# Optimization experiments

Measured on AMD Instinct MI355X. Metric: run time of the kernel, lower is better.

## Reference

```python
import jax, jax.numpy as jnp
import numpy as np


def _layernorm(x, w, b):
    mu = x.mean(-1, keepdims=True)
    var = ((x - mu) ** 2).mean(-1, keepdims=True)
    return (x - mu) * jax.lax.rsqrt(var + 1e-5) * w + b


def _s5_scan(u, Lam, Bc, Cc, D, log_step):
    # Diagonal S5 SSM, ZOH discretization, parallel associative scan over time.
    step = jnp.exp(log_step)                       # (P,)
    Lbar = jnp.exp(Lam * step)                     # (P,) complex
    Bbar = ((Lbar - 1.0) / Lam)[:, None] * Bc      # (P,H) complex
    Bu = jnp.einsum('ph,blh->blp', Bbar, u.astype(Bbar.dtype))  # (B,L,P)
    Le = jnp.broadcast_to(Lbar, Bu.shape)

    def binop(e1, e2):
        a1, b1 = e1
        a2, b2 = e2
        return a1 * a2, a2 * b1 + b2

    _, xs = jax.lax.associative_scan(binop, (Le, Bu), axis=1)   # hidden states (B,L,P)
    return 2.0 * jnp.einsum('hp,blp->blh', Cc, xs).real + D * u


def _s5_block(x, ln1_w, ln1_b, Lam_re, Lam_im, B_re, B_im, C_re, C_im, D, log_step,
              ln2_w, ln2_b, ff_enc_w, ff_dec_w):
    # S5Block.forward (dropout = identity at inference)
    fx = _layernorm(x, ln1_w, ln1_b)
    Lam = -jnp.exp(Lam_re) + 1j * Lam_im           # stable-real parametrization
    y = _s5_scan(fx, Lam, B_re + 1j * B_im, C_re + 1j * C_im, D, log_step)
    x = jax.nn.gelu(y, approximate=False) + fx
    fx = _layernorm(x, ln2_w, ln2_b)
    h = fx @ ff_enc_w                              # (B,L,2N) -> GEGLU
    v, g = jnp.split(h, 2, axis=-1)
    h = v * jax.nn.gelu(g, approximate=False)
    return h @ ff_dec_w + fx


def reference(z_input, dt, ln1_w, ln1_b, Lam_re, Lam_im, B_re, B_im, C_re, C_im, D,
              log_step, ln2_w, ln2_b, ff_enc_w, ff_dec_w, toA_w1, toA_b1, toA_w2,
              toA_b2, mask_A):
    Bsz, L, N = z_input.shape
    x = z_input
    for i in range(ln1_w.shape[0]):                # n_ssmlayer_A stacked S5 blocks
        x = _s5_block(x, ln1_w[i], ln1_b[i], Lam_re[i], Lam_im[i], B_re[i], B_im[i],
                      C_re[i], C_im[i], D[i], log_step[i], ln2_w[i], ln2_b[i],
                      ff_enc_w[i], ff_dec_w[i])
    # ssm_to_A: Linear -> Softplus -> Linear
    h = jax.nn.softplus(x @ toA_w1 + toA_b1)
    Unk_A = h @ toA_w2 + toA_b2                    # (B,L,N*N)
    # SSM_step_ODE.get_seq_dynamics with A_known_const = 0
    A = Unk_A.reshape(Bsz, L, N, N) * mask_A
    # bilinear (Tustin) discretization: A_bar = (I - dt/2 A)^-1 (I + dt/2 A)
    I = jnp.eye(N, dtype=A.dtype)
    dtA = 0.5 * dt[..., None, None] * A
    A_bar = jnp.linalg.solve(I - dtA, I + dtA)     # (B,L,N,N)
    # roll latent state through the discretized dynamics
    z0 = z_input[:, 0]

    def step(z, Ab):
        z2 = jnp.einsum('bij,bj->bi', Ab, z)
        return z2, z2

    _, ys = jax.lax.scan(step, z0, jnp.moveaxis(A_bar[:, :-1], 1, 0))
    traj = jnp.concatenate([z0[None], ys], axis=0)  # (L,B,N)
    return jnp.moveaxis(traj, 0, 1)                 # (B,L,N)


def setup_inputs() -> dict:
    key = jax.random.key(0)
    ks = jax.random.split(key, 16)
    B, L, N, P, NL, H = 32, 512, 64, 128, 2, 128
    d = {}
    d['z_input'] = jax.random.normal(ks[0], (B, L, N), jnp.float32)
    d['dt'] = jax.random.uniform(ks[1], (B, L), jnp.float32) * 0.01
    d['ln1_w'] = jnp.ones((NL, N), jnp.float32)
    d['ln1_b'] = jnp.zeros((NL, N), jnp.float32)
    d['Lam_re'] = jax.random.normal(ks[2], (NL, P), jnp.float32) * 0.5
    d['Lam_im'] = jax.random.normal(ks[3], (NL, P), jnp.float32) * np.pi
    d['B_re'] = jax.random.normal(ks[4], (NL, P, N), jnp.float32) / np.sqrt(N)
    d['B_im'] = jax.random.normal(ks[5], (NL, P, N), jnp.float32) / np.sqrt(N)
    d['C_re'] = jax.random.normal(ks[6], (NL, N, P), jnp.float32) / np.sqrt(P)
    d['C_im'] = jax.random.normal(ks[7], (NL, N, P), jnp.float32) / np.sqrt(P)
    d['D'] = jax.random.normal(ks[8], (NL, N), jnp.float32)
    lo, hi = np.log(1e-3), np.log(1e-1)
    d['log_step'] = lo + jax.random.uniform(ks[9], (NL, P), jnp.float32) * (hi - lo)
    d['ln2_w'] = jnp.ones((NL, N), jnp.float32)
    d['ln2_b'] = jnp.zeros((NL, N), jnp.float32)
    d['ff_enc_w'] = jax.random.normal(ks[10], (NL, N, 2 * N), jnp.float32) / np.sqrt(N)
    d['ff_dec_w'] = jax.random.normal(ks[11], (NL, N, N), jnp.float32) / np.sqrt(N)
    d['toA_w1'] = jax.random.normal(ks[12], (N, H), jnp.float32) * 0.1
    d['toA_b1'] = jnp.zeros((H,), jnp.float32)
    d['toA_w2'] = jax.random.normal(ks[13], (H, N * N), jnp.float32) * 0.002
    d['toA_b2'] = jnp.zeros((N * N,), jnp.float32)
    d['mask_A'] = jnp.ones((N, N), jnp.float32)
    return d
```

## Files before the change

### kernel.cpp

```cpp
#include <hip/hip_runtime.h>

#define DI __device__ __forceinline__

typedef unsigned short u16;
typedef unsigned int u32;
typedef __attribute__((ext_vector_type(8))) short shortx8;
typedef __attribute__((ext_vector_type(4))) float floatx4;

DI float u2f(u32 x) { union { u32 u; float f; } v; v.u = x; return v.f; }
DI u32 f2u(float x) { union { u32 u; float f; } v; v.f = x; return v.u; }
DI float bflo(u32 w) { return u2f(w << 16); }
DI float bfhi(u32 w) { return u2f(w & 0xffff0000u); }
DI float bf1(u16 w) { return u2f(((u32)w) << 16); }
DI u16 f2bf(float f) {
  u32 u = f2u(f);
  u32 r = (u + 0x7fffu + ((u >> 16) & 1u)) >> 16;
  return (u16)r;
}

DI float wsum64(float v) {
  v += __shfl_xor(v, 32);
  v += __shfl_xor(v, 16);
  v += __shfl_xor(v, 8);
  v += __shfl_xor(v, 4);
  v += __shfl_xor(v, 2);
  v += __shfl_xor(v, 1);
  return v;
}

DI float gelu_ex(float y) { return 0.5f * y * (1.0f + erff(y * 0.7071067811865476f)); }
DI float softplus_ex(float x) { return x > 0.f ? x + log1pf(expf(-x)) : log1pf(expf(x)); }

__global__ void k_pre(const float* __restrict__ Lam_re, const float* __restrict__ Lam_im,
                      const float* __restrict__ log_step,
                      const float* __restrict__ B_re, const float* __restrict__ B_im,
                      const float* __restrict__ C_re, const float* __restrict__ C_im,
                      float* __restrict__ wLbar, float* __restrict__ wBbr, float* __restrict__ wBbi,
                      float* __restrict__ wCtr, float* __restrict__ wCti) {
  int l = blockIdx.x;
  int p = threadIdx.x;
  int idx = l * 128 + p;
  float step = expf(log_step[idx]);
  float lre = -expf(Lam_re[idx]);
  float lim = Lam_im[idx];
  float er = expf(lre * step);
  float Lr = er * cosf(lim * step);
  float Li = er * sinf(lim * step);
  wLbar[idx * 2] = Lr;
  wLbar[idx * 2 + 1] = Li;
  float inv = 1.0f / (lre * lre + lim * lim);
  float nr = Lr - 1.0f, ni = Li;
  float qr = (nr * lre + ni * lim) * inv;
  float qi = (ni * lre - nr * lim) * inv;
  for (int h = 0; h < 64; ++h) {
    float br = B_re[idx * 64 + h], bim = B_im[idx * 64 + h];
    wBbr[(l * 64 + h) * 128 + p] = qr * br - qi * bim;
    wBbi[(l * 64 + h) * 128 + p] = qr * bim + qi * br;
    wCtr[idx * 64 + h] = C_re[(l * 64 + h) * 128 + p];
    wCti[idx * 64 + h] = C_im[(l * 64 + h) * 128 + p];
  }
}

__global__ __launch_bounds__(256) void k_prew(const float* __restrict__ w2, u16* __restrict__ w2T) {
  __shared__ float s[128][65];
  int t = threadIdx.x;
  int n0 = blockIdx.x * 64;
  for (int i = 0; i < 32; ++i) {
    int e = i * 256 + t;
    int k = e >> 6, n = e & 63;
    s[k][n] = w2[(size_t)k * 4096 + n0 + n];
  }
  __syncthreads();
  for (int i = 0; i < 16; ++i) {
    int e = i * 256 + t;
    int n = e >> 6, kp = e & 63;
    u32 pk = (u32)f2bf(s[kp * 2][n]) | ((u32)f2bf(s[kp * 2 + 1][n]) << 16);
    ((u32*)w2T)[(size_t)(n0 + n) * 64 + kp] = pk;
  }
}

__global__ __launch_bounds__(256) void k_ln_bu(
    const float* __restrict__ xin, const float* __restrict__ lnw, const float* __restrict__ lnb,
    const float* __restrict__ wBbr, const float* __restrict__ wBbi,
    float* __restrict__ fxg, float2* __restrict__ bu, int layer) {
  __shared__ float sbr[64 * 128];
  __shared__ float sbi[64 * 128];
  int t = threadIdx.x, w = t >> 6, lane = t & 63;
  {
    const float* br = wBbr + (size_t)layer * 8192;
    const float* bi = wBbi + (size_t)layer * 8192;
    for (int e = t; e < 8192; e += 256) { sbr[e] = br[e]; sbi[e] = bi[e]; }
  }
  float wv = lnw[layer * 64 + lane], bv = lnb[layer * 64 + lane];
  __syncthreads();
  int row0 = blockIdx.x * 32 + w * 8;
  float fxv[8];
#pragma unroll
  for (int rr = 0; rr < 8; ++rr) {
    size_t r = row0 + rr;
    float x = xin[r * 64 + lane];
    float mu = wsum64(x) * 0.015625f;
    float d = x - mu;
    float var = wsum64(d * d) * 0.015625f;
    float fx = d * rsqrtf(var + 1e-5f) * wv + bv;
    fxv[rr] = fx;
    fxg[r * 64 + lane] = fx;
  }
  float ar0[8] = {}, ai0[8] = {}, ar1[8] = {}, ai1[8] = {};
  for (int h = 0; h < 64; ++h) {
    float b0r = sbr[h * 128 + lane], b0i = sbi[h * 128 + lane];
    float b1r = sbr[h * 128 + lane + 64], b1i = sbi[h * 128 + lane + 64];
#pragma unroll
    for (int rr = 0; rr < 8; ++rr) {
      float f = __shfl(fxv[rr], h);
      ar0[rr] = fmaf(b0r, f, ar0[rr]);
      ai0[rr] = fmaf(b0i, f, ai0[rr]);
      ar1[rr] = fmaf(b1r, f, ar1[rr]);
      ai1[rr] = fmaf(b1i, f, ai1[rr]);
    }
  }
#pragma unroll
  for (int rr = 0; rr < 8; ++rr) {
    size_t r = row0 + rr;
    bu[r * 128 + lane] = make_float2(ar0[rr], ai0[rr]);
    bu[r * 128 + lane + 64] = make_float2(ar1[rr], ai1[rr]);
  }
}

__global__ __launch_bounds__(256) void k_scan(float2* __restrict__ bu,
                                              const float* __restrict__ wLbar, int layer) {
  __shared__ float2 carry[16][17];
  int t = threadIdx.x;
  int ck = t >> 4, chain = t & 15;
  int b = blockIdx.x >> 3;
  int p = (blockIdx.x & 7) * 16 + chain;
  float Lr = wLbar[(layer * 128 + p) * 2];
  float Li = wLbar[(layer * 128 + p) * 2 + 1];
  float2* ptr = bu + ((size_t)b * 512 * 128 + p);
  int l0 = ck * 32;
  float xr = 0.f, xi = 0.f;
#pragma unroll 4
  for (int i = 0; i < 32; ++i) {
    float2 v = ptr[(size_t)(l0 + i) * 128];
    float nr = fmaf(Lr, xr, fmaf(-Li, xi, v.x));
    float ni = fmaf(Lr, xi, fmaf(Li, xr, v.y));
    xr = nr; xi = ni;
  }
  carry[chain][ck] = make_float2(xr, xi);
  __syncthreads();
  if (t < 16) {
    float ar = Lr, ai = Li;
#pragma unroll
    for (int s = 0; s < 5; ++s) {
      float nr = ar * ar - ai * ai;
      float ni = 2.f * ar * ai;
      ar = nr; ai = ni;
    }
    float cr = 0.f, ci2 = 0.f;
#pragma unroll
    for (int m = 0; m < 16; ++m) {
      float2 loc = carry[t][m];
      carry[t][m] = make_float2(cr, ci2);
      float nr = fmaf(ar, cr, fmaf(-ai, ci2, loc.x));
      float ni = fmaf(ar, ci2, fmaf(ai, cr, loc.y));
      cr = nr; ci2 = ni;
    }
  }
  __syncthreads();
  float2 c0 = carry[chain][ck];
  xr = c0.x; xi = c0.y;
#pragma unroll 4
  for (int i = 0; i < 32; ++i) {
    float2 v = ptr[(size_t)(l0 + i) * 128];
    float nr = fmaf(Lr, xr, fmaf(-Li, xi, v.x));
    float ni = fmaf(Lr, xi, fmaf(Li, xr, v.y));
    xr = nr; xi = ni;
    ptr[(size_t)(l0 + i) * 128] = make_float2(xr, xi);
  }
}

__global__ __launch_bounds__(256) void k_yproj(
    const float2* __restrict__ xs, const float* __restrict__ wCtr, const float* __restrict__ wCti,
    const float* __restrict__ fxg, const float* __restrict__ Dp,
    float* __restrict__ xout, int layer) {
  __shared__ float ctr[64 * 64];
  __shared__ float cti[64 * 64];
  __shared__ float2 xsh[4][8][64];
  int t = threadIdx.x, w = t >> 6, lane = t & 63;
  int row0 = blockIdx.x * 32 + w * 8;
  float acc[8] = {};
  for (int ph = 0; ph < 2; ++ph) {
    __syncthreads();
    {
      const float* sr = wCtr + ((size_t)layer * 128 + ph * 64) * 64;
      const float* si = wCti + ((size_t)layer * 128 + ph * 64) * 64;
      for (int e = t; e < 4096; e += 256) { ctr[e] = sr[e]; cti[e] = si[e]; }
    }
#pragma unroll
    for (int rr = 0; rr < 8; ++rr) {
      size_t r = row0 + rr;
      xsh[w][rr][lane] = xs[r * 128 + ph * 64 + lane];
    }
    __syncthreads();
    for (int p = 0; p < 64; ++p) {
      float cr = ctr[p * 64 + lane];
      float ci = cti[p * 64 + lane];
#pragma unroll
      for (int rr = 0; rr < 8; ++rr) {
        float2 xv = xsh[w][rr][p];
        acc[rr] = fmaf(cr, xv.x, fmaf(-ci, xv.y, acc[rr]));
      }
    }
  }
  float Dv = Dp[layer * 64 + lane];
#pragma unroll
  for (int rr = 0; rr < 8; ++rr) {
    size_t r = row0 + rr;
    float u = fxg[r * 64 + lane];
    float y = 2.f * acc[rr] + Dv * u;
    xout[r * 64 + lane] = gelu_ex(y) + u;
  }
}

__global__ __launch_bounds__(256) void k_ff(
    float* __restrict__ xio, const float* __restrict__ lnw, const float* __restrict__ lnb,
    const float* __restrict__ encw, const float* __restrict__ decw, int layer) {
  __shared__ float enc[64 * 128];
  __shared__ float dec[64 * 64];
  int t = threadIdx.x, w = t >> 6, lane = t & 63;
  {
    const float* e = encw + (size_t)layer * 8192;
    for (int i = t; i < 8192; i += 256) enc[i] = e[i];
    const float* d = decw + (size_t)layer * 4096;
    for (int i = t; i < 4096; i += 256) dec[i] = d[i];
  }
  float wv = lnw[layer * 64 + lane], bv = lnb[layer * 64 + lane];
  __syncthreads();
  int row0 = blockIdx.x * 32 + w * 8;
  float fx2v[8];
#pragma unroll
  for (int rr = 0; rr < 8; ++rr) {
    size_t r = row0 + rr;
    float x = xio[r * 64 + lane];
    float mu = wsum64(x) * 0.015625f;
    float d = x - mu;
    float var = wsum64(d * d) * 0.015625f;
    fx2v[rr] = d * rsqrtf(var + 1e-5f) * wv + bv;
  }
  float h0[8] = {}, h1v[8] = {};
  for (int h = 0; h < 64; ++h) {
    float e0 = enc[h * 128 + lane], e1 = enc[h * 128 + lane + 64];
#pragma unroll
    for (int rr = 0; rr < 8; ++rr) {
      float f = __shfl(fx2v[rr], h);
      h0[rr] = fmaf(e0, f, h0[rr]);
      h1v[rr] = fmaf(e1, f, h1v[rr]);
    }
  }
  float gv[8];
#pragma unroll
  for (int rr = 0; rr < 8; ++rr) gv[rr] = h0[rr] * gelu_ex(h1v[rr]);
  float o[8] = {};
  for (int j = 0; j < 64; ++j) {
    float dv = dec[j * 64 + lane];
#pragma unroll
    for (int rr = 0; rr < 8; ++rr) {
      float gj = __shfl(gv[rr], j);
      o[rr] = fmaf(dv, gj, o[rr]);
    }
  }
#pragma unroll
  for (int rr = 0; rr < 8; ++rr) {
    size_t r = row0 + rr;
    xio[r * 64 + lane] = o[rr] + fx2v[rr];
  }
}

__global__ __launch_bounds__(256) void k_toa1(
    const float* __restrict__ xin, const float* __restrict__ w1, const float* __restrict__ b1,
    u16* __restrict__ h1out) {
  __shared__ float w1s[64 * 128];
  int t = threadIdx.x, w = t >> 6, lane = t & 63;
  for (int i = t; i < 8192; i += 256) w1s[i] = w1[i];
  float bb0 = b1[lane], bb1 = b1[lane + 64];
  __syncthreads();
  int row0 = blockIdx.x * 32 + w * 8;
  float xv[8];
#pragma unroll
  for (int rr = 0; rr < 8; ++rr) xv[rr] = xin[(size_t)(row0 + rr) * 64 + lane];
  float a0[8] = {}, a1[8] = {};
  for (int h = 0; h < 64; ++h) {
    float e0 = w1s[h * 128 + lane], e1 = w1s[h * 128 + lane + 64];
#pragma unroll
    for (int rr = 0; rr < 8; ++rr) {
      float f = __shfl(xv[rr], h);
      a0[rr] = fmaf(e0, f, a0[rr]);
      a1[rr] = fmaf(e1, f, a1[rr]);
    }
  }
#pragma unroll
  for (int rr = 0; rr < 8; ++rr) {
    size_t r = row0 + rr;
    float v0 = softplus_ex(a0[rr] + bb0);
    float v1 = softplus_ex(a1[rr] + bb1);
    int sl = (2 * lane) & 63;
    float ea = __shfl(v0, sl), eb = __shfl(v1, sl);
    float oa = __shfl(v0, sl + 1), ob = __shfl(v1, sl + 1);
    float lo = (lane < 32) ? ea : eb;
    float hi = (lane < 32) ? oa : ob;
    ((u32*)h1out)[r * 64 + lane] = (u32)f2bf(lo) | ((u32)f2bf(hi) << 16);
  }
}

__global__ __launch_bounds__(256) void k_gemm_mfma(
    const u16* __restrict__ w2T,
    const u16* __restrict__ h1,
    const float* __restrict__ b2, const float* __restrict__ mask,
    const float* __restrict__ dt, u16* __restrict__ Xout) {
  __shared__ __align__(16) u16 As[128 * 128];
  __shared__ __align__(16) u16 Bs[128 * 128];
  int t = threadIdx.x;
  int bn = blockIdx.x;
  int bm = blockIdx.y;
  {
    const u16* srcA = w2T + (size_t)(bn * 128) * 128;
    const u16* srcB = h1 + (size_t)(bm * 128) * 128;
#pragma unroll
    for (int i = 0; i < 8; ++i) {
      int r = i * 16 + (t >> 4);
      int gs = t & 15;
      int gsw = (gs & 8) | ((gs ^ r) & 7);
      uint4 va = *(const uint4*)(srcA + r * 128 + gs * 8);
      *(uint4*)(As + r * 128 + gsw * 8) = va;
      uint4 vb = *(const uint4*)(srcB + r * 128 + gs * 8);
      *(uint4*)(Bs + r * 128 + gsw * 8) = vb;
    }
  }
  __syncthreads();
  int w = t >> 6, l = t & 63;
  int n0 = (w & 1) * 64, m0 = (w >> 1) * 64;
  int lr = l & 15, kg = l >> 4;
  floatx4 acc[4][4];
#pragma unroll
  for (int i = 0; i < 4; ++i)
#pragma unroll
    for (int j = 0; j < 4; ++j) acc[i][j] = (floatx4){0.f, 0.f, 0.f, 0.f};
#pragma unroll
  for (int kk = 0; kk < 4; ++kk) {
    int g = kk * 4 + kg;
    shortx8 af[4], bf[4];
#pragma unroll
    for (int ni = 0; ni < 4; ++ni) {
      int r = n0 + ni * 16 + lr;
      int gsw = (g & 8) | ((g ^ r) & 7);
      af[ni] = *(const shortx8*)(As + r * 128 + gsw * 8);
    }
#pragma unroll
    for (int mi = 0; mi < 4; ++mi) {
      int r = m0 + mi * 16 + lr;
      int gsw = (g & 8) | ((g ^ r) & 7);
      bf[mi] = *(const shortx8*)(Bs + r * 128 + gsw * 8);
    }
#pragma unroll
    for (int ni = 0; ni < 4; ++ni)
#pragma unroll
      for (int mi = 0; mi < 4; ++mi)
        acc[ni][mi] = __builtin_amdgcn_mfma_f32_16x16x32_bf16(af[ni], bf[mi], acc[ni][mi], 0, 0, 0);
  }
  __syncthreads();
  int q = (l >> 4) * 4;
#pragma unroll
  for (int mi = 0; mi < 4; ++mi) {
    int ml = m0 + mi * 16 + lr;
    int m = bm * 128 + ml;
    float dv = 0.5f * dt[m];
#pragma unroll
    for (int ni = 0; ni < 4; ++ni) {
      int nl = n0 + ni * 16 + q;
      int n = bn * 128 + nl;
      float4 bb = *(const float4*)&b2[n];
      float4 mk = *(const float4*)&mask[n];
      floatx4 a = acc[ni][mi];
      float x0 = dv * (a[0] + bb.x) * mk.x;
      float x1 = dv * (a[1] + bb.y) * mk.y;
      float x2 = dv * (a[2] + bb.z) * mk.z;
      float x3 = dv * (a[3] + bb.w) * mk.w;
      u32 lo = (u32)f2bf(x0) | ((u32)f2bf(x1) << 16);
      u32 hi = (u32)f2bf(x2) | ((u32)f2bf(x3) << 16);
      int g = nl >> 3;
      int gsw = (g & 8) | ((g ^ ml) & 7);
      *(uint2*)(As + ml * 128 + gsw * 8 + (nl & 7)) = make_uint2(lo, hi);
    }
  }
  __syncthreads();
  int seg = t & 7;
#pragma unroll
  for (int pp = 0; pp < 4; ++pp) {
    int r = pp * 32 + (t >> 3);
#pragma unroll
    for (int ii = 0; ii < 2; ++ii) {
      int g = seg * 2 + ii;
      int gsw = (g & 8) | ((g ^ r) & 7);
      uint4 v = *(const uint4*)(As + r * 128 + gsw * 8);
      *(uint4*)&Xout[(size_t)(bm * 128 + r) * 4096 + bn * 128 + g * 8] = v;
    }
  }
}

__global__ __launch_bounds__(256, 4) void k_chunk(u16* __restrict__ Xg) {
  __shared__ __align__(16) u16 Xrm[4096];
  __shared__ __align__(16) u16 XTrm[4096];
  __shared__ __align__(16) u16 Erm[4096];
  __shared__ __align__(16) u16 STb[4096];
  __shared__ __align__(16) u16 SOut[4096];
  int t = threadIdx.x, w = t >> 6, l = t & 63;
  int lr = l & 15, kg = l >> 4;
  int b = blockIdx.x >> 5, c = blockIdx.x & 31;
  u16* base = Xg + ((size_t)(b * 512 + c * 16)) * 4096;
  floatx4 sreg[4];
#pragma unroll
  for (int i = 0; i < 4; ++i) sreg[i] = (floatx4){0.f, 0.f, 0.f, 0.f};
  int r0 = (t >> 3) * 2, c0 = (t & 7) * 8, g0 = t & 7;
  int cw = t >> 3;
  uint4 pf0 = *(const uint4*)(base + r0 * 64 + c0);
  uint4 pf1 = *(const uint4*)(base + (r0 + 1) * 64 + c0);
  int q0 = w * 16 + kg * 4;
  int qrow = w * 16 + lr;
  int wr = t >> 2, wg = (t & 3) * 2;
  for (int j = 0; j < 16; ++j) {
    __syncthreads();
    if (j > 0) {
      u16* Xprev = base + (size_t)(j - 1) * 4096;
      uint4 v0 = *(const uint4*)(SOut + wr * 64 + (((wg + 0) ^ wr) & 7) * 8);
      uint4 v1 = *(const uint4*)(SOut + wr * 64 + (((wg + 1) ^ wr) & 7) * 8);
      *(uint4*)(Xprev + wr * 64 + wg * 8) = v0;
      *(uint4*)(Xprev + wr * 64 + wg * 8 + 8) = v1;
    }
    *(uint4*)(Xrm + r0 * 64 + ((g0 ^ r0) & 7) * 8) = pf0;
    *(uint4*)(Xrm + (r0 + 1) * 64 + ((g0 ^ (r0 + 1)) & 7) * 8) = pf1;
    {
      const u16* a = (const u16*)&pf0;
      const u16* bq = (const u16*)&pf1;
#pragma unroll
      for (int i = 0; i < 8; ++i) {
        int ci = (i + t) & 7;
        int cc = c0 + ci;
        u32 val = (u32)a[ci] | ((u32)bq[ci] << 16);
        ((u32*)XTrm)[cc * 32 + (((cw >> 2) ^ cc) & 7) * 4 + (cw & 3)] = val;
      }
    }
#pragma unroll
    for (int j2 = 0; j2 < 4; ++j2) {
      int p = j2 * 16 + lr;
      floatx4 s = sreg[j2];
      float v0 = s[0] + ((p == q0 + 0) ? 1.f : 0.f);
      float v1 = s[1] + ((p == q0 + 1) ? 1.f : 0.f);
      float v2 = s[2] + ((p == q0 + 2) ? 1.f : 0.f);
      float v3 = s[3] + ((p == q0 + 3) ? 1.f : 0.f);
      u32 lo = (u32)f2bf(v0) | ((u32)f2bf(v1) << 16);
      u32 hi = (u32)f2bf(v2) | ((u32)f2bf(v3) << 16);
      *(uint2*)(STb + p * 64 + (((q0 >> 3) ^ p) & 7) * 8 + (q0 & 7)) = make_uint2(lo, hi);
    }
    if (j < 15) {
      const u16* nx = base + (size_t)(j + 1) * 4096;
      pf0 = *(const uint4*)(nx + r0 * 64 + c0);
      pf1 = *(const uint4*)(nx + (r0 + 1) * 64 + c0);
    }
    __syncthreads();
    shortx8 afx0 = *(const shortx8*)(XTrm + qrow * 64 + ((kg ^ qrow) & 7) * 8);
    shortx8 afx1 = *(const shortx8*)(XTrm + qrow * 64 + (((4 + kg) ^ qrow) & 7) * 8);
    {
      floatx4 acc[4];
#pragma unroll
      for (int i = 0; i < 4; ++i) acc[i] = (floatx4){0.f, 0.f, 0.f, 0.f};
#pragma unroll
      for (int kk = 0; kk < 2; ++kk) {
        int g = kk * 4 + kg;
        shortx8 af = kk ? afx1 : afx0;
#pragma unroll
        for (int j2 = 0; j2 < 4; ++j2) {
          int p = j2 * 16 + lr;
          shortx8 bf = *(const shortx8*)(Xrm + p * 64 + ((g ^ p) & 7) * 8);
          acc[j2] = __builtin_amdgcn_mfma_f32_16x16x32_bf16(af, bf, acc[j2], 0, 0, 0);
        }
      }
#pragma unroll
      for (int j2 = 0; j2 < 4; ++j2) {
        int p = j2 * 16 + lr;
        int sw = (((q0 >> 3) ^ p) & 7) * 8 + (q0 & 7);
        uint2 xv = *(const uint2*)(Xrm + p * 64 + sw);
        floatx4 a = acc[j2];
        float e0 = 2.f * (bflo(xv.x) + a[0]);
        float e1 = 2.f * (bfhi(xv.x) + a[1]);
        float e2 = 2.f * (bflo(xv.y) + a[2]);
        float e3 = 2.f * (bfhi(xv.y) + a[3]);
        u32 lo = (u32)f2bf(e0) | ((u32)f2bf(e1) << 16);
        u32 hi = (u32)f2bf(e2) | ((u32)f2bf(e3) << 16);
        *(uint2*)(Erm + p * 64 + sw) = make_uint2(lo, hi);
      }
    }
    __syncthreads();
    {
      floatx4 acc[4];
#pragma unroll
      for (int i = 0; i < 4; ++i) acc[i] = (floatx4){0.f, 0.f, 0.f, 0.f};
#pragma unroll
      for (int kk = 0; kk < 2; ++kk) {
        int g = kk * 4 + kg;
        shortx8 af = *(const shortx8*)(Erm + qrow * 64 + ((g ^ qrow) & 7) * 8);
#pragma unroll
        for (int j2 = 0; j2 < 4; ++j2) {
          int p = j2 * 16 + lr;
          shortx8 bf = *(const shortx8*)(STb + p * 64 + ((g ^ p) & 7) * 8);
          acc[j2] = __builtin_amdgcn_mfma_f32_16x16x32_bf16(af, bf, acc[j2], 0, 0, 0);
        }
      }
#pragma unroll
      for (int j2 = 0; j2 < 4; ++j2) {
        int p = j2 * 16 + lr;
        floatx4 a = acc[j2];
        floatx4 s = sreg[j2];
        s[0] += a[0]; s[1] += a[1]; s[2] += a[2]; s[3] += a[3];
        sreg[j2] = s;
        u32 lo = (u32)f2bf(s[0]) | ((u32)f2bf(s[1]) << 16);
        u32 hi = (u32)f2bf(s[2]) | ((u32)f2bf(s[3]) << 16);
        *(uint2*)(SOut + p * 64 + (((q0 >> 3) ^ p) & 7) * 8 + (q0 & 7)) = make_uint2(lo, hi);
      }
    }
  }
  __syncthreads();
  {
    u16* Xprev = base + (size_t)15 * 4096;
    uint4 v0 = *(const uint4*)(SOut + wr * 64 + (((wg + 0) ^ wr) & 7) * 8);
    uint4 v1 = *(const uint4*)(SOut + wr * 64 + (((wg + 1) ^ wr) & 7) * 8);
    *(uint4*)(Xprev + wr * 64 + wg * 8) = v0;
    *(uint4*)(Xprev + wr * 64 + wg * 8 + 8) = v1;
  }
}

__global__ __launch_bounds__(64) void k_carry(const float* __restrict__ zin,
                                              const u16* __restrict__ R,
                                              float* __restrict__ out) {
  __shared__ __align__(16) u16 Ms[2][4096];
  int b = blockIdx.x, l = threadIdx.x;
  {
    const u16* M0 = R + ((size_t)(b * 512 + 15)) * 4096;
#pragma unroll
    for (int i = 0; i < 8; ++i) ((uint4*)Ms[0])[i * 64 + l] = ((const uint4*)M0)[i * 64 + l];
  }
  float cz = zin[(size_t)b * 512 * 64 + l];
  for (int c = 0; c < 32; ++c) {
    out[((size_t)(b * 512 + c * 16)) * 64 + l] = cz;
    uint4 nf0, nf1, nf2, nf3, nf4, nf5, nf6, nf7;
    if (c < 31) {
      const u16* Mn = R + ((size_t)(b * 512 + (c + 1) * 16 + 15)) * 4096;
      nf0 = ((const uint4*)Mn)[0 * 64 + l];
      nf1 = ((const uint4*)Mn)[1 * 64 + l];
      nf2 = ((const uint4*)Mn)[2 * 64 + l];
      nf3 = ((const uint4*)Mn)[3 * 64 + l];
      nf4 = ((const uint4*)Mn)[4 * 64 + l];
      nf5 = ((const uint4*)Mn)[5 * 64 + l];
      nf6 = ((const uint4*)Mn)[6 * 64 + l];
      nf7 = ((const uint4*)Mn)[7 * 64 + l];
    }
    const u16* M = Ms[c & 1];
    float a0 = 0.f, a1 = 0.f, a2 = 0.f, a3 = 0.f;
#pragma unroll
    for (int k = 0; k < 64; k += 4) {
      a0 = fmaf(bf1(M[(k + 0) * 64 + l]), __shfl(cz, k + 0), a0);
      a1 = fmaf(bf1(M[(k + 1) * 64 + l]), __shfl(cz, k + 1), a1);
      a2 = fmaf(bf1(M[(k + 2) * 64 + l]), __shfl(cz, k + 2), a2);
      a3 = fmaf(bf1(M[(k + 3) * 64 + l]), __shfl(cz, k + 3), a3);
    }
    cz += (a0 + a1) + (a2 + a3);
    if (c < 31) {
      uint4* d = (uint4*)Ms[(c + 1) & 1];
      d[0 * 64 + l] = nf0; d[1 * 64 + l] = nf1; d[2 * 64 + l] = nf2; d[3 * 64 + l] = nf3;
      d[4 * 64 + l] = nf4; d[5 * 64 + l] = nf5; d[6 * 64 + l] = nf6; d[7 * 64 + l] = nf7;
    }
  }
}

__global__ __launch_bounds__(256) void k_apply(const u16* __restrict__ R,
                                               float* __restrict__ out) {
  __shared__ float carr[64];
  int t = threadIdx.x, w = t >> 6, l = t & 63;
  int b = blockIdx.x >> 5, c = blockIdx.x & 31;
  const u16* Rb = R + ((size_t)(b * 512 + c * 16)) * 4096;
  if (t < 64) carr[t] = out[((size_t)(b * 512 + c * 16)) * 64 + t];
  __syncthreads();
  for (int j = w; j < 15; j += 4) {
    const u16* M = Rb + (size_t)j * 4096;
    float a0 = 0.f, a1 = 0.f, a2 = 0.f, a3 = 0.f;
#pragma unroll
    for (int k = 0; k < 64; k += 4) {
      a0 = fmaf(bf1(M[(k + 0) * 64 + l]), carr[k + 0], a0);
      a1 = fmaf(bf1(M[(k + 1) * 64 + l]), carr[k + 1], a1);
      a2 = fmaf(bf1(M[(k + 2) * 64 + l]), carr[k + 2], a2);
      a3 = fmaf(bf1(M[(k + 3) * 64 + l]), carr[k + 3], a3);
    }
    float zo = carr[l] + ((a0 + a1) + (a2 + a3));
    out[((size_t)(b * 512 + c * 16 + j + 1)) * 64 + l] = zo;
  }
}

extern "C" void kernel_launch(void* const* d_in, const int* in_sizes, int n_in,
                              void* d_out, int out_size, void* d_ws, size_t ws_size,
                              hipStream_t stream) {
  const float* z_input  = (const float*)d_in[0];
  const float* dt       = (const float*)d_in[1];
  const float* ln1_w    = (const float*)d_in[2];
  const float* ln1_b    = (const float*)d_in[3];
  const float* Lam_re   = (const float*)d_in[4];
  const float* Lam_im   = (const float*)d_in[5];
  const float* B_re     = (const float*)d_in[6];
  const float* B_im     = (const float*)d_in[7];
  const float* C_re     = (const float*)d_in[8];
  const float* C_im     = (const float*)d_in[9];
  const float* Dp       = (const float*)d_in[10];
  const float* log_step = (const float*)d_in[11];
  const float* ln2_w    = (const float*)d_in[12];
  const float* ln2_b    = (const float*)d_in[13];
  const float* ff_enc   = (const float*)d_in[14];
  const float* ff_dec   = (const float*)d_in[15];
  const float* toA_w1   = (const float*)d_in[16];
  const float* toA_b1   = (const float*)d_in[17];
  const float* toA_w2   = (const float*)d_in[18];
  const float* toA_b2   = (const float*)d_in[19];
  const float* mask_A   = (const float*)d_in[20];

  char* ws = (char*)d_ws;
  float* wLbar = (float*)(ws + 0);
  float* wBbr  = (float*)(ws + 2048);
  float* wBbi  = (float*)(ws + 67584);
  float* wCtr  = (float*)(ws + 133120);
  float* wCti  = (float*)(ws + 198656);
  float* wfx   = (float*)(ws + 264192);
  float* wx    = (float*)(ws + 4458496);
  float2* wbu  = (float2*)(ws + 8652800);
  u16* wh1     = (u16*)(ws + 25430016);
  u16* w2T     = (u16*)(ws + 29624320);
  u16* wX      = (u16*)(ws + 30672896);
  if (ws_size < 164890624ull) return;

  k_pre<<<2, 128, 0, stream>>>(Lam_re, Lam_im, log_step, B_re, B_im, C_re, C_im,
                               wLbar, wBbr, wBbi, wCtr, wCti);
  k_prew<<<64, 256, 0, stream>>>(toA_w2, w2T);
  for (int l = 0; l < 2; ++l) {
    const float* xin = (l == 0) ? z_input : wx;
    k_ln_bu<<<512, 256, 0, stream>>>(xin, ln1_w, ln1_b, wBbr, wBbi, wfx, wbu, l);
    k_scan<<<256, 256, 0, stream>>>(wbu, wLbar, l);
    k_yproj<<<512, 256, 0, stream>>>(wbu, wCtr, wCti, wfx, Dp, wx, l);
    k_ff<<<512, 256, 0, stream>>>(wx, ln2_w, ln2_b, ff_enc, ff_dec, l);
  }
  k_toa1<<<512, 256, 0, stream>>>(wx, toA_w1, toA_b1, wh1);
  k_gemm_mfma<<<dim3(32, 128), 256, 0, stream>>>(w2T, wh1, toA_b2, mask_A, dt, wX);
  k_chunk<<<1024, 256, 0, stream>>>(wX);
  k_carry<<<32, 64, 0, stream>>>(z_input, wX, (float*)d_out);
  k_apply<<<1024, 256, 0, stream>>>(wX, (float*)d_out);
}
```

Before: 396.9 us.

## Fuse y-projection, feed-forward and toA1 kernels; merge prep kernels; register-resident carry matrices

Merges the two preprocessing kernels into one launch. Fuses the y-projection, FF block and (for the last layer) the first toA linear layer into a single kernel, with a shared-memory union. This removes intermediate global round-trips and several launches. The carry and apply kernels now read matrices with row-wise vector loads into registers instead of staging through shared memory, and the chunk kernel's output store is changed from packed to scalar transposed writes, which changes the stored layout and could slow that store path.

New measurement: 387.0 us. 1.03x faster.

```diff
diff --git a/kernel.cpp b/kernel.cpp
--- a/kernel.cpp
+++ b/kernel.cpp
@@ -31,51 +31,55 @@
 DI float gelu_ex(float y) { return 0.5f * y * (1.0f + erff(y * 0.7071067811865476f)); }
 DI float softplus_ex(float x) { return x > 0.f ? x + log1pf(expf(-x)) : log1pf(expf(x)); }
 
-__global__ void k_pre(const float* __restrict__ Lam_re, const float* __restrict__ Lam_im,
-                      const float* __restrict__ log_step,
-                      const float* __restrict__ B_re, const float* __restrict__ B_im,
-                      const float* __restrict__ C_re, const float* __restrict__ C_im,
-                      float* __restrict__ wLbar, float* __restrict__ wBbr, float* __restrict__ wBbi,
-                      float* __restrict__ wCtr, float* __restrict__ wCti) {
-  int l = blockIdx.x;
-  int p = threadIdx.x;
-  int idx = l * 128 + p;
-  float step = expf(log_step[idx]);
-  float lre = -expf(Lam_re[idx]);
-  float lim = Lam_im[idx];
-  float er = expf(lre * step);
-  float Lr = er * cosf(lim * step);
-  float Li = er * sinf(lim * step);
-  wLbar[idx * 2] = Lr;
-  wLbar[idx * 2 + 1] = Li;
-  float inv = 1.0f / (lre * lre + lim * lim);
-  float nr = Lr - 1.0f, ni = Li;
-  float qr = (nr * lre + ni * lim) * inv;
-  float qi = (ni * lre - nr * lim) * inv;
-  for (int h = 0; h < 64; ++h) {
-    float br = B_re[idx * 64 + h], bim = B_im[idx * 64 + h];
-    wBbr[(l * 64 + h) * 128 + p] = qr * br - qi * bim;
-    wBbi[(l * 64 + h) * 128 + p] = qr * bim + qi * br;
-    wCtr[idx * 64 + h] = C_re[(l * 64 + h) * 128 + p];
-    wCti[idx * 64 + h] = C_im[(l * 64 + h) * 128 + p];
-  }
-}
-
-__global__ __launch_bounds__(256) void k_prew(const float* __restrict__ w2, u16* __restrict__ w2T) {
-  __shared__ float s[128][65];
-  int t = threadIdx.x;
-  int n0 = blockIdx.x * 64;
-  for (int i = 0; i < 32; ++i) {
-    int e = i * 256 + t;
-    int k = e >> 6, n = e & 63;
-    s[k][n] = w2[(size_t)k * 4096 + n0 + n];
-  }
-  __syncthreads();
-  for (int i = 0; i < 16; ++i) {
-    int e = i * 256 + t;
-    int n = e >> 6, kp = e & 63;
-    u32 pk = (u32)f2bf(s[kp * 2][n]) | ((u32)f2bf(s[kp * 2 + 1][n]) << 16);
-    ((u32*)w2T)[(size_t)(n0 + n) * 64 + kp] = pk;
+__global__ __launch_bounds__(256) void k_pre2(
+    const float* __restrict__ Lam_re, const float* __restrict__ Lam_im,
+    const float* __restrict__ log_step,
+    const float* __restrict__ B_re, const float* __restrict__ B_im,
+    const float* __restrict__ C_re, const float* __restrict__ C_im,
+    const float* __restrict__ w2,
+    float* __restrict__ wLbar, float* __restrict__ wBbr, float* __restrict__ wBbi,
+    float* __restrict__ wCtr, float* __restrict__ wCti, u16* __restrict__ w2T) {
+  if (blockIdx.x < 64) {
+    __shared__ float s[128][65];
+    int t = threadIdx.x;
+    int n0 = blockIdx.x * 64;
+    for (int i = 0; i < 32; ++i) {
+      int e = i * 256 + t;
+      int k = e >> 6, n = e & 63;
+      s[k][n] = w2[(size_t)k * 4096 + n0 + n];
+    }
+    __syncthreads();
+    for (int i = 0; i < 16; ++i) {
+      int e = i * 256 + t;
+      int n = e >> 6, kp = e & 63;
+      u32 pk = (u32)f2bf(s[kp * 2][n]) | ((u32)f2bf(s[kp * 2 + 1][n]) << 16);
+      ((u32*)w2T)[(size_t)(n0 + n) * 64 + kp] = pk;
+    }
+  } else {
+    int l = blockIdx.x - 64;
+    int p = threadIdx.x;
+    if (p < 128) {
+      int idx = l * 128 + p;
+      float step = expf(log_step[idx]);
+      float lre = -expf(Lam_re[idx]);
+      float lim = Lam_im[idx];
+      float er = expf(lre * step);
+      float Lr = er * cosf(lim * step);
+      float Li = er * sinf(lim * step);
+      wLbar[idx * 2] = Lr;
+      wLbar[idx * 2 + 1] = Li;
+      float inv = 1.0f / (lre * lre + lim * lim);
+      float nr = Lr - 1.0f, ni = Li;
+      float qr = (nr * lre + ni * lim) * inv;
+      float qi = (ni * lre - nr * lim) * inv;
+      for (int h = 0; h < 64; ++h) {
+        float br = B_re[idx * 64 + h], bim = B_im[idx * 64 + h];
+        wBbr[(l * 64 + h) * 128 + p] = qr * br - qi * bim;
+        wBbi[(l * 64 + h) * 128 + p] = qr * bim + qi * br;
+        wCtr[idx * 64 + h] = C_re[(l * 64 + h) * 128 + p];
+        wCti[idx * 64 + h] = C_im[(l * 64 + h) * 128 + p];
+      }
+    }
   }
 }
 
@@ -179,13 +183,18 @@
   }
 }
 
-__global__ __launch_bounds__(256) void k_yproj(
+__global__ __launch_bounds__(256) void k_yff(
     const float2* __restrict__ xs, const float* __restrict__ wCtr, const float* __restrict__ wCti,
     const float* __restrict__ fxg, const float* __restrict__ Dp,
-    float* __restrict__ xout, int layer) {
-  __shared__ float ctr[64 * 64];
-  __shared__ float cti[64 * 64];
-  __shared__ float2 xsh[4][8][64];
+    const float* __restrict__ ln2w, const float* __restrict__ ln2b,
+    const float* __restrict__ encw, const float* __restrict__ decw,
+    const float* __restrict__ w1, const float* __restrict__ b1,
+    float* __restrict__ xout, u16* __restrict__ h1out, int layer) {
+  __shared__ union {
+    struct { float ctr[4096]; float cti[4096]; float2 xsh[4][8][64]; } a;
+    struct { float enc[8192]; float dec[4096]; } b;
+    struct { float w1s[8192]; } c;
+  } sm;
   int t = threadIdx.x, w = t >> 6, lane = t & 63;
   int row0 = blockIdx.x * 32 + w * 8;
   float acc[8] = {};
@@ -194,54 +203,46 @@
     {
       const float* sr = wCtr + ((size_t)layer * 128 + ph * 64) * 64;
       const float* si = wCti + ((size_t)layer * 128 + ph * 64) * 64;
-      for (int e = t; e < 4096; e += 256) { ctr[e] = sr[e]; cti[e] = si[e]; }
+      for (int e = t; e < 4096; e += 256) { sm.a.ctr[e] = sr[e]; sm.a.cti[e] = si[e]; }
     }
 #pragma unroll
     for (int rr = 0; rr < 8; ++rr) {
       size_t r = row0 + rr;
-      xsh[w][rr][lane] = xs[r * 128 + ph * 64 + lane];
+      sm.a.xsh[w][rr][lane] = xs[r * 128 + ph * 64 + lane];
     }
     __syncthreads();
     for (int p = 0; p < 64; ++p) {
-      float cr = ctr[p * 64 + lane];
-      float ci = cti[p * 64 + lane];
+      float cr = sm.a.ctr[p * 64 + lane];
+      float ci = sm.a.cti[p * 64 + lane];
 #pragma unroll
       for (int rr = 0; rr < 8; ++rr) {
-        float2 xv = xsh[w][rr][p];
+        float2 xv = sm.a.xsh[w][rr][p];
         acc[rr] = fmaf(cr, xv.x, fmaf(-ci, xv.y, acc[rr]));
       }
     }
   }
   float Dv = Dp[layer * 64 + lane];
+  float xv[8];
 #pragma unroll
   for (int rr = 0; rr < 8; ++rr) {
     size_t r = row0 + rr;
     float u = fxg[r * 64 + lane];
     float y = 2.f * acc[rr] + Dv * u;
-    xout[r * 64 + lane] = gelu_ex(y) + u;
-  }
-}
-
-__global__ __launch_bounds__(256) void k_ff(
-    float* __restrict__ xio, const float* __restrict__ lnw, const float* __restrict__ lnb,
-    const float* __restrict__ encw, const float* __restrict__ decw, int layer) {
-  __shared__ float enc[64 * 128];
-  __shared__ float dec[64 * 64];
-  int t = threadIdx.x, w = t >> 6, lane = t & 63;
+    xv[rr] = gelu_ex(y) + u;
+  }
+  __syncthreads();
   {
     const float* e = encw + (size_t)layer * 8192;
-    for (int i = t; i < 8192; i += 256) enc[i] = e[i];
+    for (int i = t; i < 8192; i += 256) sm.b.enc[i] = e[i];
     const float* d = decw + (size_t)layer * 4096;
-    for (int i = t; i < 4096; i += 256) dec[i] = d[i];
-  }
-  float wv = lnw[layer * 64 + lane], bv = lnb[layer * 64 + lane];
-  __syncthreads();
-  int row0 = blockIdx.x * 32 + w * 8;
+    for (int i = t; i < 4096; i += 256) sm.b.dec[i] = d[i];
+  }
+  float wv = ln2w[layer * 64 + lane], bv = ln2b[layer * 64 + lane];
+  __syncthreads();
   float fx2v[8];
 #pragma unroll
   for (int rr = 0; rr < 8; ++rr) {
-    size_t r = row0 + rr;
-    float x = xio[r * 64 + lane];
+    float x = xv[rr];
     float mu = wsum64(x) * 0.015625f;
     float d = x - mu;
     float var = wsum64(d * d) * 0.015625f;
@@ -249,7 +250,7 @@
   }
   float h0[8] = {}, h1v[8] = {};
   for (int h = 0; h < 64; ++h) {
-    float e0 = enc[h * 128 + lane], e1 = enc[h * 128 + lane + 64];
+    float e0 = sm.b.enc[h * 128 + lane], e1 = sm.b.enc[h * 128 + lane + 64];
 #pragma unroll
     for (int rr = 0; rr < 8; ++rr) {
       float f = __shfl(fx2v[rr], h);
@@ -260,40 +261,35 @@
   float gv[8];
 #pragma unroll
   for (int rr = 0; rr < 8; ++rr) gv[rr] = h0[rr] * gelu_ex(h1v[rr]);
-  float o[8] = {};
-  for (int j = 0; j < 64; ++j) {
-    float dv = dec[j * 64 + lane];
-#pragma unroll
-    for (int rr = 0; rr < 8; ++rr) {
-      float gj = __shfl(gv[rr], j);
-      o[rr] = fmaf(dv, gj, o[rr]);
-    }
-  }
-#pragma unroll
-  for (int rr = 0; rr < 8; ++rr) {
-    size_t r = row0 + rr;
-    xio[r * 64 + lane] = o[rr] + fx2v[rr];
-  }
-}
-
-__global__ __launch_bounds__(256) void k_toa1(
-    const float* __restrict__ xin, const float* __restrict__ w1, const float* __restrict__ b1,
-    u16* __restrict__ h1out) {
-  __shared__ float w1s[64 * 128];
-  int t = threadIdx.x, w = t >> 6, lane = t & 63;
-  for (int i = t; i < 8192; i += 256) w1s[i] = w1[i];
+  float x2[8];
+  {
+    float o[8] = {};
+    for (int j = 0; j < 64; ++j) {
+      float dv = sm.b.dec[j * 64 + lane];
+#pragma unroll
+      for (int rr = 0; rr < 8; ++rr) {
+        float gj = __shfl(gv[rr], j);
+        o[rr] = fmaf(dv, gj, o[rr]);
+      }
+    }
+#pragma unroll
+    for (int rr = 0; rr < 8; ++rr) x2[rr] = o[rr] + fx2v[rr];
+  }
+  if (layer == 0) {
+#pragma unroll
+    for (int rr = 0; rr < 8; ++rr) xout[(size_t)(row0 + rr) * 64 + lane] = x2[rr];
+    return;
+  }
+  __syncthreads();
+  for (int i = t; i < 8192; i += 256) sm.c.w1s[i] = w1[i];
   float bb0 = b1[lane], bb1 = b1[lane + 64];
   __syncthreads();
-  int row0 = blockIdx.x * 32 + w * 8;
-  float xv[8];
-#pragma unroll
-  for (int rr = 0; rr < 8; ++rr) xv[rr] = xin[(size_t)(row0 + rr) * 64 + lane];
   float a0[8] = {}, a1[8] = {};
   for (int h = 0; h < 64; ++h) {
-    float e0 = w1s[h * 128 + lane], e1 = w1s[h * 128 + lane + 64];
+    float e0 = sm.c.w1s[h * 128 + lane], e1 = sm.c.w1s[h * 128 + lane + 64];
 #pragma unroll
     for (int rr = 0; rr < 8; ++rr) {
-      float f = __shfl(xv[rr], h);
+      float f = __shfl(x2[rr], h);
       a0[rr] = fmaf(e0, f, a0[rr]);
       a1[rr] = fmaf(e1, f, a1[rr]);
     }
@@ -313,8 +309,7 @@
 }
 
 __global__ __launch_bounds__(256) void k_gemm_mfma(
-    const u16* __restrict__ w2T,
-    const u16* __restrict__ h1,
+    const u16* __restrict__ w2T, const u16* __restrict__ h1,
     const float* __restrict__ b2, const float* __restrict__ mask,
     const float* __restrict__ dt, u16* __restrict__ Xout) {
   __shared__ __align__(16) u16 As[128 * 128];
@@ -522,9 +517,11 @@
         floatx4 s = sreg[j2];
         s[0] += a[0]; s[1] += a[1]; s[2] += a[2]; s[3] += a[3];
         sreg[j2] = s;
-        u32 lo = (u32)f2bf(s[0]) | ((u32)f2bf(s[1]) << 16);
-        u32 hi = (u32)f2bf(s[2]) | ((u32)f2bf(s[3]) << 16);
-        *(uint2*)(SOut + p * 64 + (((q0 >> 3) ^ p) & 7) * 8 + (q0 & 7)) = make_uint2(lo, hi);
+#pragma unroll
+        for (int i = 0; i < 4; ++i) {
+          int r2 = q0 + i;
+          SOut[r2 * 64 + (((p >> 3) ^ r2) & 7) * 8 + (p & 7)] = f2bf(s[i]);
+        }
       }
     }
   }
@@ -541,42 +538,39 @@
 __global__ __launch_bounds__(64) void k_carry(const float* __restrict__ zin,
                                               const u16* __restrict__ R,
                                               float* __restrict__ out) {
-  __shared__ __align__(16) u16 Ms[2][4096];
   int b = blockIdx.x, l = threadIdx.x;
+  uint4 cf[8], nf[8];
   {
-    const u16* M0 = R + ((size_t)(b * 512 + 15)) * 4096;
-#pragma unroll
-    for (int i = 0; i < 8; ++i) ((uint4*)Ms[0])[i * 64 + l] = ((const uint4*)M0)[i * 64 + l];
+    const uint4* M0 = (const uint4*)(R + ((size_t)(b * 512 + 15)) * 4096 + l * 64);
+#pragma unroll
+    for (int g = 0; g < 8; ++g) cf[g] = M0[g];
   }
   float cz = zin[(size_t)b * 512 * 64 + l];
   for (int c = 0; c < 32; ++c) {
     out[((size_t)(b * 512 + c * 16)) * 64 + l] = cz;
-    uint4 nf0, nf1, nf2, nf3, nf4, nf5, nf6, nf7;
     if (c < 31) {
-      const u16* Mn = R + ((size_t)(b * 512 + (c + 1) * 16 + 15)) * 4096;
-      nf0 = ((const uint4*)Mn)[0 * 64 + l];
-      nf1 = ((const uint4*)Mn)[1 * 64 + l];
-      nf2 = ((const uint4*)Mn)[2 * 64 + l];
-      nf3 = ((const uint4*)Mn)[3 * 64 + l];
-      nf4 = ((const uint4*)Mn)[4 * 64 + l];
-      nf5 = ((const uint4*)Mn)[5 * 64 + l];
-      nf6 = ((const uint4*)Mn)[6 * 64 + l];
-      nf7 = ((const uint4*)Mn)[7 * 64 + l];
-    }
-    const u16* M = Ms[c & 1];
+      const uint4* Mn = (const uint4*)(R + ((size_t)(b * 512 + (c + 1) * 16 + 15)) * 4096 + l * 64);
+#pragma unroll
+      for (int g = 0; g < 8; ++g) nf[g] = Mn[g];
+    }
     float a0 = 0.f, a1 = 0.f, a2 = 0.f, a3 = 0.f;
 #pragma unroll
-    for (int k = 0; k < 64; k += 4) {
-      a0 = fmaf(bf1(M[(k + 0) * 64 + l]), __shfl(cz, k + 0), a0);
-      a1 = fmaf(bf1(M[(k + 1) * 64 + l]), __shfl(cz, k + 1), a1);
-      a2 = fmaf(bf1(M[(k + 2) * 64 + l]), __shfl(cz, k + 2), a2);
-      a3 = fmaf(bf1(M[(k + 3) * 64 + l]), __shfl(cz, k + 3), a3);
+    for (int g = 0; g < 8; ++g) {
+      uint4 v = cf[g];
+      int k = g * 8;
+      a0 = fmaf(bflo(v.x), __shfl(cz, k + 0), a0);
+      a1 = fmaf(bfhi(v.x), __shfl(cz, k + 1), a1);
+      a2 = fmaf(bflo(v.y), __shfl(cz, k + 2), a2);
+      a3 = fmaf(bfhi(v.y), __shfl(cz, k + 3), a3);
+      a0 = fmaf(bflo(v.z), __shfl(cz, k + 4), a0);
+      a1 = fmaf(bfhi(v.z), __shfl(cz, k + 5), a1);
+      a2 = fmaf(bflo(v.w), __shfl(cz, k + 6), a2);
+      a3 = fmaf(bfhi(v.w), __shfl(cz, k + 7), a3);
     }
     cz += (a0 + a1) + (a2 + a3);
     if (c < 31) {
-      uint4* d = (uint4*)Ms[(c + 1) & 1];
-      d[0 * 64 + l] = nf0; d[1 * 64 + l] = nf1; d[2 * 64 + l] = nf2; d[3 * 64 + l] = nf3;
-      d[4 * 64 + l] = nf4; d[5 * 64 + l] = nf5; d[6 * 64 + l] = nf6; d[7 * 64 + l] = nf7;
+#pragma unroll
+      for (int g = 0; g < 8; ++g) cf[g] = nf[g];
     }
   }
 }
@@ -589,18 +583,24 @@
   const u16* Rb = R + ((size_t)(b * 512 + c * 16)) * 4096;
   if (t < 64) carr[t] = out[((size_t)(b * 512 + c * 16)) * 64 + t];
   __syncthreads();
+  float zl = carr[l];
   for (int j = w; j < 15; j += 4) {
-    const u16* M = Rb + (size_t)j * 4096;
+    const uint4* M = (const uint4*)(Rb + (size_t)j * 4096 + l * 64);
     float a0 = 0.f, a1 = 0.f, a2 = 0.f, a3 = 0.f;
 #pragma unroll
-    for (int k = 0; k < 64; k += 4) {
-      a0 = fmaf(bf1(M[(k + 0) * 64 + l]), carr[k + 0], a0);
-      a1 = fmaf(bf1(M[(k + 1) * 64 + l]), carr[k + 1], a1);
-      a2 = fmaf(bf1(M[(k + 2) * 64 + l]), carr[k + 2], a2);
-      a3 = fmaf(bf1(M[(k + 3) * 64 + l]), carr[k + 3], a3);
-    }
-    float zo = carr[l] + ((a0 + a1) + (a2 + a3));
-    out[((size_t)(b * 512 + c * 16 + j + 1)) * 64 + l] = zo;
+    for (int g = 0; g < 8; ++g) {
+      uint4 v = M[g];
+      const float* zb = &carr[g * 8];
+      a0 = fmaf(bflo(v.x), zb[0], a0);
+      a1 = fmaf(bfhi(v.x), zb[1], a1);
+      a2 = fmaf(bflo(v.y), zb[2], a2);
+      a3 = fmaf(bfhi(v.y), zb[3], a3);
+      a0 = fmaf(bflo(v.z), zb[4], a0);
+      a1 = fmaf(bfhi(v.z), zb[5], a1);
+      a2 = fmaf(bflo(v.w), zb[6], a2);
+      a3 = fmaf(bfhi(v.w), zb[7], a3);
+    }
+    out[((size_t)(b * 512 + c * 16 + j + 1)) * 64 + l] = zl + ((a0 + a1) + (a2 + a3));
   }
 }
 
@@ -643,17 +643,15 @@
   u16* wX      = (u16*)(ws + 30672896);
   if (ws_size < 164890624ull) return;
 
-  k_pre<<<2, 128, 0, stream>>>(Lam_re, Lam_im, log_step, B_re, B_im, C_re, C_im,
-                               wLbar, wBbr, wBbi, wCtr, wCti);
-  k_prew<<<64, 256, 0, stream>>>(toA_w2, w2T);
+  k_pre2<<<66, 256, 0, stream>>>(Lam_re, Lam_im, log_step, B_re, B_im, C_re, C_im,
+                                 toA_w2, wLbar, wBbr, wBbi, wCtr, wCti, w2T);
   for (int l = 0; l < 2; ++l) {
     const float* xin = (l == 0) ? z_input : wx;
     k_ln_bu<<<512, 256, 0, stream>>>(xin, ln1_w, ln1_b, wBbr, wBbi, wfx, wbu, l);
     k_scan<<<256, 256, 0, stream>>>(wbu, wLbar, l);
-    k_yproj<<<512, 256, 0, stream>>>(wbu, wCtr, wCti, wfx, Dp, wx, l);
-    k_ff<<<512, 256, 0, stream>>>(wx, ln2_w, ln2_b, ff_enc, ff_dec, l);
-  }
-  k_toa1<<<512, 256, 0, stream>>>(wx, toA_w1, toA_b1, wh1);
+    k_yff<<<512, 256, 0, stream>>>(wbu, wCtr, wCti, wfx, Dp, ln2_w, ln2_b, ff_enc, ff_dec,
+                                   toA_w1, toA_b1, wx, wh1, l);
+  }
   k_gemm_mfma<<<dim3(32, 128), 256, 0, stream>>>(w2T, wh1, toA_b2, mask_A, dt, wX);
   k_chunk<<<1024, 256, 0, stream>>>(wX);
   k_carry<<<32, 64, 0, stream>>>(z_input, wX, (float*)d_out);
```
